# Kernel tuning notes

Hardware: AMD Instinct MI355X
Metric: run time of the kernel (lower is better)

The kernel has to match this reference:

```python
import jax, jax.numpy as jnp
import numpy as np

B, S, D, H = 2, 2048, 1024, 16
DK = D // H  # 64


def setup_inputs() -> dict:
    key = jax.random.key(0)
    ks = jax.random.split(key, 4)
    scale = 1.0 / np.sqrt(D)
    return {
        "q_input": jax.random.normal(ks[0], (B, S, D), dtype=jnp.float32),
        "W_q": jax.random.normal(ks[1], (D, D), dtype=jnp.float32) * scale,
        "b_q": jnp.zeros((D,), dtype=jnp.float32),
        "W_k": jax.random.normal(ks[2], (D, D), dtype=jnp.float32) * scale,
        "b_k": jnp.zeros((D,), dtype=jnp.float32),
        "W_v": jax.random.normal(ks[3], (D, D), dtype=jnp.float32) * scale,
        "b_v": jnp.zeros((D,), dtype=jnp.float32),
    }


def reference(q_input, W_q, b_q, W_k, b_k, W_v, b_v):
    # Self-attention: k_input and v_input default to q_input in the torch module.
    # nn.Linear computes x @ W.T + b
    q = q_input @ W_q.T + b_q
    k = q_input @ W_k.T + b_k
    v = q_input @ W_v.T + b_v

    # [B,S,D] -> [B,H,S,DK]
    def split_heads(x):
        return x.reshape(B, S, H, DK).transpose(0, 2, 1, 3)

    qh, kh, vh = split_heads(q), split_heads(k), split_heads(v)

    # scores [B,H,S,S]; causal mask added BEFORE scaling (as in source; -inf invariant)
    scores = jnp.einsum("bhqd,bhkd->bhqk", qh, kh)
    causal = jnp.tril(jnp.ones((S, S), dtype=bool))
    scores = jnp.where(causal[None, None], scores, -jnp.inf)
    scores = scores / jnp.sqrt(jnp.float32(DK))
    probs = jax.nn.softmax(scores, axis=-1)
    z = jnp.einsum("bhqk,bhkd->bhqd", probs, vh)  # [B,H,S,DK]
    # [B,H,S,DK] -> [B,S,H,DK] -> [B,S,D]
    return z.transpose(0, 2, 1, 3).reshape(B, S, D)
```

## Files before the change

kernel.cpp:

```cpp
#include <hip/hip_runtime.h>
#include <hip/hip_bf16.h>
#include <stdint.h>

typedef __attribute__((ext_vector_type(8))) short short8;
typedef __attribute__((ext_vector_type(4))) short short4v;
typedef __attribute__((ext_vector_type(4))) float f32x4;

#define B_ 2
#define S_ 2048
#define D_ 1024
#define H_ 16
#define DK_ 64
#define M_ (B_*S_)

#define WS_QKV   0
#define WS_XB    12582912
#define WS_WB    16777216

#define QSCALE (0.125f * 1.44269504088896f)

#define GLL16(g, l) __builtin_amdgcn_global_load_lds( \
    (const __attribute__((address_space(1))) void*)(g), \
    (__attribute__((address_space(3))) void*)(l), 16, 0, 0)

#define WAIT_VM0 asm volatile("s_waitcnt vmcnt(0)" ::: "memory")
#define WAIT_VM4 asm volatile("s_waitcnt vmcnt(4)" ::: "memory")
#define BARRIER_RAW asm volatile("s_barrier" ::: "memory")

static __device__ __forceinline__ short f2bf(float f){
  union { float f; unsigned u; } x; x.f = f;
  unsigned r = x.u + 0x7fff + ((x.u >> 16) & 1);
  return (short)(r >> 16);
}

__global__ __launch_bounds__(256) void cvt_bf16(
    const float* __restrict__ X,  const float* __restrict__ Wq,
    const float* __restrict__ Wk, const float* __restrict__ Wv,
    short* __restrict__ ws)
{
  const int z = blockIdx.z;
  const float* src; short* dst; int n;
  if (z == 0)      { src = X;  dst = ws + WS_XB;               n = M_*D_; }
  else if (z == 1) { src = Wq; dst = ws + WS_WB;               n = D_*D_; }
  else if (z == 2) { src = Wk; dst = ws + WS_WB + D_*D_;       n = D_*D_; }
  else             { src = Wv; dst = ws + WS_WB + 2*(D_*D_);   n = D_*D_; }
  const int stride = gridDim.x * blockDim.x * 4;
  for (int i = (blockIdx.x * blockDim.x + threadIdx.x) * 4; i < n; i += stride) {
    float4 v = *(const float4*)(src + i);
    short4v o;
    o.x = f2bf(v.x); o.y = f2bf(v.y); o.z = f2bf(v.z); o.w = f2bf(v.w);
    *(short4v*)(dst + i) = o;
  }
}

__global__ __launch_bounds__(256, 3) void qkv_gemm(
    const short* __restrict__ ws_in,
    const float* __restrict__ bq, const float* __restrict__ bk,
    const float* __restrict__ bv, short* __restrict__ qkv)
{
  const int z = blockIdx.z;
  const short* X  = ws_in + WS_XB;
  const short* Wm = ws_in + WS_WB + (size_t)z * (D_*D_);
  const float* bias = (z==0) ? bq : (z==1) ? bk : bv;
  short* out = qkv + (size_t)z * (M_*D_);

  __shared__ short lds[24576];

  const int t = threadIdx.x;
  const int w = t >> 6, lane = t & 63;
  const int quad = lane >> 4, l16 = lane & 15;
  const int wm = w & 1, wn = w >> 1;
  const int m0 = blockIdx.y * 128, n0 = blockIdx.x * 128;

  const int lr = lane >> 2, lc = lane & 3;
  const int csrc = lc ^ (lr & 3);
  const size_t arow0 = (size_t)(m0 + w*16     + lr) * D_ + csrc*8;
  const size_t arow1 = (size_t)(m0 + (w+4)*16 + lr) * D_ + csrc*8;
  const size_t brow0 = (size_t)(n0 + w*16     + lr) * D_ + csrc*8;
  const size_t brow1 = (size_t)(n0 + (w+4)*16 + lr) * D_ + csrc*8;

  f32x4 acc[4][4];
  #pragma unroll
  for (int i=0;i<4;i++)
    #pragma unroll
    for (int j=0;j<4;j++) acc[i][j] = (f32x4){0.f,0.f,0.f,0.f};

  #pragma unroll
  for (int p=0;p<2;p++){
    GLL16(X  + arow0 + p*32, lds + p*4096 + (w*16)*32);
    GLL16(X  + arow1 + p*32, lds + p*4096 + ((w+4)*16)*32);
    GLL16(Wm + brow0 + p*32, lds + 12288 + p*4096 + (w*16)*32);
    GLL16(Wm + brow1 + p*32, lds + 12288 + p*4096 + ((w+4)*16)*32);
  }

  const int ca = quad ^ (l16 & 3);
  int cur = 0;
  for (int kk = 0; kk < 32; kk++) {
    if (kk < 31) { WAIT_VM4; }
    else         { WAIT_VM0; }
    BARRIER_RAW;
    if (kk < 30) {
      int slot = cur + 2; if (slot >= 3) slot -= 3;
      const int ko = (kk+2)*32;
      short* An = lds + slot*4096;
      short* Bn = lds + 12288 + slot*4096;
      GLL16(X  + arow0 + ko, An + (w*16)*32);
      GLL16(X  + arow1 + ko, An + ((w+4)*16)*32);
      GLL16(Wm + brow0 + ko, Bn + (w*16)*32);
      GLL16(Wm + brow1 + ko, Bn + ((w+4)*16)*32);
    }
    const short* Ac = lds + cur*4096;
    const short* Bc = lds + 12288 + cur*4096;
    short8 af[4], bfr[4];
    #pragma unroll
    for (int mt=0;mt<4;mt++)
      af[mt] = *(const short8*)(Ac + (wm*64 + mt*16 + l16)*32 + ca*8);
    #pragma unroll
    for (int nt=0;nt<4;nt++)
      bfr[nt] = *(const short8*)(Bc + (wn*64 + nt*16 + l16)*32 + ca*8);
    if (z != 2) {
      #pragma unroll
      for (int mt=0;mt<4;mt++)
        #pragma unroll
        for (int nt=0;nt<4;nt++)
          acc[mt][nt] = __builtin_amdgcn_mfma_f32_16x16x32_bf16(af[mt], bfr[nt], acc[mt][nt], 0,0,0);
    } else {
      #pragma unroll
      for (int nt=0;nt<4;nt++)
        #pragma unroll
        for (int mt=0;mt<4;mt++)
          acc[nt][mt] = __builtin_amdgcn_mfma_f32_16x16x32_bf16(bfr[nt], af[mt], acc[nt][mt], 0,0,0);
    }
    cur = (cur==2) ? 0 : cur+1;
  }

  __syncthreads();

  if (z != 2) {
    const float scale = (z==0) ? QSCALE : 1.0f;
    #pragma unroll
    for (int nt=0;nt<4;nt++){
      const int col_l = wn*64 + nt*16 + l16;
      const float bvv = bias[n0 + col_l];
      #pragma unroll
      for (int mt=0;mt<4;mt++)
        #pragma unroll
        for (int i=0;i<4;i++){
          const int row_l = wm*64 + mt*16 + quad*4 + i;
          lds[row_l*136 + col_l] = f2bf((acc[mt][nt][i] + bvv) * scale);
        }
    }
    __syncthreads();
    #pragma unroll
    for (int k=0;k<8;k++){
      const int cid = k*256 + t;
      const int row = cid >> 4, cc = cid & 15;
      short8 vv = *(const short8*)(lds + row*136 + cc*8);
      const int m = m0 + row, bidx = m >> 11, s = m & 2047;
      const int n = n0 + cc*8, h = n >> 6, dd = n & 63;
      *(short8*)(out + (((size_t)(bidx*H_ + h))*S_ + s)*DK_ + dd) = vv;
    }
  } else {
    #pragma unroll
    for (int nt=0;nt<4;nt++)
      #pragma unroll
      for (int i=0;i<4;i++){
        const int n_l = wn*64 + nt*16 + quad*4 + i;
        const float bvv = bias[n0 + n_l];
        #pragma unroll
        for (int mt=0;mt<4;mt++){
          const int m_l = wm*64 + mt*16 + l16;
          lds[n_l*136 + m_l] = f2bf(acc[nt][mt][i] + bvv);
        }
      }
    __syncthreads();
    #pragma unroll
    for (int k=0;k<8;k++){
      const int cid = k*256 + t;
      const int rowN = cid >> 4, cc = cid & 15;
      short8 vv = *(const short8*)(lds + rowN*136 + cc*8);
      const int n = n0 + rowN, h = n >> 6, dd = n & 63;
      const int m = m0 + cc*8, bidx = m >> 11, s0 = m & 2047;
      *(short8*)(out + (((size_t)(bidx*H_ + h))*DK_ + dd)*S_ + s0) = vv;
    }
  }
}

__global__ __launch_bounds__(256, 2) void attn(
    const short* __restrict__ qkv, float* __restrict__ out)
{
  const int bh = blockIdx.y;
  const int qt = (gridDim.x - 1) - blockIdx.x;
  const short* Q  = qkv + (size_t)bh * (S_*DK_);
  const short* K  = Q + (size_t)(M_*D_);
  const short* VT = qkv + (size_t)(2*M_*D_) + (size_t)bh * (DK_*S_);

  __shared__ short Qs[8192];
  __shared__ short Kbuf[2][4096];
  __shared__ short Vbuf[2][4096];
  __shared__ short Ps[8192];

  const int t = threadIdx.x;
  const int w = t >> 6, lane = t & 63;
  const int quad = lane >> 4, l16 = lane & 15;
  const int sw = l16 & 7;
  const int lr = lane >> 3, lc = lane & 7;
  const int csrc = lc ^ lr;

  #pragma unroll
  for (int p=0;p<4;p++){
    const int rb = (p*4 + w)*8;
    GLL16(Q + (size_t)(qt*128 + rb + lr)*DK_ + csrc*8, Qs + rb*64);
  }
  #pragma unroll
  for (int j=0;j<2;j++){
    const int rb = (j*4 + w)*8;
    GLL16(K  + (size_t)(rb + lr)*DK_ + csrc*8, &Kbuf[0][0] + rb*64);
    GLL16(VT + (size_t)(rb + lr)*S_  + csrc*8, &Vbuf[0][0] + rb*64);
  }

  f32x4 o[2][4];
  float lsum[2];
  #pragma unroll
  for (int mt=0;mt<2;mt++){
    #pragma unroll
    for (int nd=0;nd<4;nd++) o[mt][nd] = (f32x4){0.f,0.f,0.f,0.f};
    lsum[mt] = 0.f;
  }

  short8 bq[2][2];
  const int nkt = 2*qt + 2;
  int cur = 0;
  const int pw_half = (quad & 1) * 4;
  const int pw_ckb  = quad >> 1;

  for (int kt = 0; kt < nkt; kt++){
    WAIT_VM0;
    BARRIER_RAW;
    const int nxt = cur ^ 1;
    if (kt + 1 < nkt) {
      const int kb2 = (kt+1)*64;
      short* Kn = &Kbuf[nxt][0];
      short* Vn = &Vbuf[nxt][0];
      #pragma unroll
      for (int j=0;j<2;j++){
        const int rb = (j*4 + w)*8;
        GLL16(K  + (size_t)(kb2 + rb + lr)*DK_ + csrc*8, Kn + rb*64);
        GLL16(VT + (size_t)(rb + lr)*S_ + kb2 + csrc*8,  Vn + rb*64);
      }
    }
    if (kt == 0) {
      #pragma unroll
      for (int kc=0;kc<2;kc++){
        const int xch = (kc*4 + quad) ^ sw;
        #pragma unroll
        for (int mt=0;mt<2;mt++)
          bq[kc][mt] = *(const short8*)(Qs + (w*32 + mt*16 + l16)*64 + xch*8);
      }
    }
    const short* Kc = &Kbuf[cur][0];
    const short* Vc = &Vbuf[cur][0];
    const int kb = kt*64;

    f32x4 sc[4][2];
    #pragma unroll
    for (int ntk=0;ntk<4;ntk++)
      #pragma unroll
      for (int mt=0;mt<2;mt++) sc[ntk][mt] = (f32x4){0.f,0.f,0.f,0.f};
    #pragma unroll
    for (int kc=0;kc<2;kc++){
      const int xch = (kc*4 + quad) ^ sw;
      short8 ak[4];
      #pragma unroll
      for (int ntk=0;ntk<4;ntk++)
        ak[ntk] = *(const short8*)(Kc + (ntk*16 + l16)*64 + xch*8);
      #pragma unroll
      for (int ntk=0;ntk<4;ntk++)
        #pragma unroll
        for (int mt=0;mt<2;mt++)
          sc[ntk][mt] = __builtin_amdgcn_mfma_f32_16x16x32_bf16(ak[ntk], bq[kc][mt], sc[ntk][mt], 0,0,0);
    }

    const int q0w = qt*128 + w*32;
    if (kb + 63 > q0w) {
      #pragma unroll
      for (int ntk=0;ntk<4;ntk++)
        #pragma unroll
        for (int mt=0;mt<2;mt++){
          const int qg = q0w + mt*16 + l16;
          #pragma unroll
          for (int i=0;i<4;i++){
            const int kg = kb + ntk*16 + quad*4 + i;
            if (kg > qg) sc[ntk][mt][i] = -3.0e38f;
          }
        }
    }

    #pragma unroll
    for (int mt=0;mt<2;mt++){
      const int r = w*32 + mt*16 + l16;
      #pragma unroll
      for (int ntk=0;ntk<4;ntk++){
        float p0 = __builtin_amdgcn_exp2f(sc[ntk][mt][0]);
        float p1 = __builtin_amdgcn_exp2f(sc[ntk][mt][1]);
        float p2 = __builtin_amdgcn_exp2f(sc[ntk][mt][2]);
        float p3 = __builtin_amdgcn_exp2f(sc[ntk][mt][3]);
        lsum[mt] += (p0+p1) + (p2+p3);
        short4v pk;
        pk.x = f2bf(p0); pk.y = f2bf(p1); pk.z = f2bf(p2); pk.w = f2bf(p3);
        const int slot = (ntk*2 + pw_ckb) ^ sw;
        *(short4v*)(Ps + r*64 + slot*8 + pw_half) = pk;
      }
    }
    asm volatile("" ::: "memory");

    #pragma unroll
    for (int kc=0;kc<2;kc++){
      const int xch = (kc*4 + quad) ^ sw;
      short8 pa[2], vb[4];
      #pragma unroll
      for (int mt=0;mt<2;mt++)
        pa[mt] = *(const short8*)(Ps + (w*32 + mt*16 + l16)*64 + xch*8);
      #pragma unroll
      for (int nd=0;nd<4;nd++)
        vb[nd] = *(const short8*)(Vc + (nd*16 + l16)*64 + xch*8);
      #pragma unroll
      for (int mt=0;mt<2;mt++)
        #pragma unroll
        for (int nd=0;nd<4;nd++)
          o[mt][nd] = __builtin_amdgcn_mfma_f32_16x16x32_bf16(pa[mt], vb[nd], o[mt][nd], 0,0,0);
    }
    cur = nxt;
  }

  const int bb = bh >> 4, h = bh & 15;
  float linv[2];
  #pragma unroll
  for (int mt=0;mt<2;mt++){
    float rs = lsum[mt];
    rs += __shfl_xor(rs, 16, 64);
    rs += __shfl_xor(rs, 32, 64);
    linv[mt] = 1.0f / rs;
  }
  #pragma unroll
  for (int mt=0;mt<2;mt++){
    #pragma unroll
    for (int i=0;i<4;i++){
      const float lw = __shfl(linv[mt], (quad<<4) + (quad<<2) + i, 64);
      const int q = qt*128 + w*32 + mt*16 + quad*4 + i;
      #pragma unroll
      for (int nd=0;nd<4;nd++){
        const int d = nd*16 + l16;
        out[ ((size_t)bb*S_ + q)*D_ + h*DK_ + d ] = o[mt][nd][i] * lw;
      }
    }
  }
}

extern "C" void kernel_launch(void* const* d_in, const int* in_sizes, int n_in,
                              void* d_out, int out_size, void* d_ws, size_t ws_size,
                              hipStream_t stream)
{
  (void)in_sizes; (void)n_in; (void)out_size; (void)ws_size;
  const float* X  = (const float*)d_in[0];
  const float* Wq = (const float*)d_in[1];
  const float* bq = (const float*)d_in[2];
  const float* Wk = (const float*)d_in[3];
  const float* bk = (const float*)d_in[4];
  const float* Wv = (const float*)d_in[5];
  const float* bv = (const float*)d_in[6];
  short* ws  = (short*)d_ws;
  float* out = (float*)d_out;

  dim3 g0(1024, 1, 4);
  cvt_bf16<<<g0, dim3(256,1,1), 0, stream>>>(X, Wq, Wk, Wv, ws);
  dim3 g1(D_/128, M_/128, 3);
  qkv_gemm<<<g1, dim3(256,1,1), 0, stream>>>(ws, bq, bk, bv, ws + WS_QKV);
  dim3 g2(S_/128, B_*H_);
  attn<<<g2, dim3(256,1,1), 0, stream>>>(ws + WS_QKV, out);
}
```

Measured before the change: 187.0 us.

## Split long causal attention rows across two blocks with atomic merge

The attention kernel now launches 24 work items per head instead of 16. For query tiles 8-15 the key range is split into two chunks of at most 16 key tiles, and the ranks are ordered so the longest work runs first. Split blocks atomically add unnormalized outputs and row sums into zeroed fp32 accumulators, and the last block to arrive normalizes and writes the result. The K/V staging also moves from double to triple buffering with a deeper prefetch. This adds a zeroing kernel, atomic traffic and reuse of workspace, in exchange for better load balance across the causal triangle.

```diff
diff --git a/kernel.cpp b/kernel.cpp
--- a/kernel.cpp
+++ b/kernel.cpp
@@ -32,6 +32,9 @@
   unsigned r = x.u + 0x7fff + ((x.u >> 16) & 1);
   return (short)(r >> 16);
 }
+
+__constant__ signed char QT_TAB[24] = {15,15,14,13,12,11,10,9,8,7,14,6,13,5,12,4,11,3,10,2,9,1,8,0};
+__constant__ signed char C_TAB[24]  = { 0, 1, 0, 0, 0, 0, 0,0,0,0, 1,0, 1,0, 1,0, 1,0, 1,0,1,0,1,0};
 
 __global__ __launch_bounds__(256) void cvt_bf16(
     const float* __restrict__ X,  const float* __restrict__ Wq,
@@ -186,19 +189,41 @@
   }
 }
 
+__global__ __launch_bounds__(256) void zero_acc(float* __restrict__ Oacc,
+                                                float* __restrict__ LT)
+{
+  const int i = blockIdx.x * 256 + threadIdx.x;
+  if (i < 524288) {
+    ((float4*)Oacc)[i] = make_float4(0.f,0.f,0.f,0.f);
+  } else {
+    const int j = i - 524288;
+    if (j < 8256) ((float4*)LT)[j] = make_float4(0.f,0.f,0.f,0.f);
+  }
+}
+
 __global__ __launch_bounds__(256, 2) void attn(
-    const short* __restrict__ qkv, float* __restrict__ out)
+    const short* __restrict__ qkv, float* __restrict__ Oacc,
+    float* __restrict__ Lacc, int* __restrict__ tick,
+    float* __restrict__ out)
 {
-  const int bh = blockIdx.y;
-  const int qt = (gridDim.x - 1) - blockIdx.x;
+  const int bh = blockIdx.x;
+  const int rank = blockIdx.y;
+  const int qt = QT_TAB[rank];
+  const int c  = C_TAB[rank];
+  const int nkt = 2*qt + 2;
+  const int kt0 = c*16;
+  const int kt1 = (kt0 + 16 < nkt) ? kt0 + 16 : nkt;
+  const bool split = (qt >= 8);
+
   const short* Q  = qkv + (size_t)bh * (S_*DK_);
   const short* K  = Q + (size_t)(M_*D_);
   const short* VT = qkv + (size_t)(2*M_*D_) + (size_t)bh * (DK_*S_);
 
   __shared__ short Qs[8192];
-  __shared__ short Kbuf[2][4096];
-  __shared__ short Vbuf[2][4096];
+  __shared__ short Kbuf[3][4096];
+  __shared__ short Vbuf[3][4096];
   __shared__ short Ps[8192];
+  __shared__ int sflag;
 
   const int t = threadIdx.x;
   const int w = t >> 6, lane = t & 63;
@@ -213,10 +238,14 @@
     GLL16(Q + (size_t)(qt*128 + rb + lr)*DK_ + csrc*8, Qs + rb*64);
   }
   #pragma unroll
-  for (int j=0;j<2;j++){
-    const int rb = (j*4 + w)*8;
-    GLL16(K  + (size_t)(rb + lr)*DK_ + csrc*8, &Kbuf[0][0] + rb*64);
-    GLL16(VT + (size_t)(rb + lr)*S_  + csrc*8, &Vbuf[0][0] + rb*64);
+  for (int p=0;p<2;p++){
+    const int kb = (kt0 + p)*64;
+    #pragma unroll
+    for (int j=0;j<2;j++){
+      const int rb = (j*4 + w)*8;
+      GLL16(K  + (size_t)(kb + rb + lr)*DK_ + csrc*8, &Kbuf[p][0] + rb*64);
+      GLL16(VT + (size_t)(rb + lr)*S_ + kb  + csrc*8, &Vbuf[p][0] + rb*64);
+    }
   }
 
   f32x4 o[2][4];
@@ -229,19 +258,18 @@
   }
 
   short8 bq[2][2];
-  const int nkt = 2*qt + 2;
-  int cur = 0;
   const int pw_half = (quad & 1) * 4;
   const int pw_ckb  = quad >> 1;
 
-  for (int kt = 0; kt < nkt; kt++){
-    WAIT_VM0;
+  for (int kt = kt0; kt < kt1; kt++){
+    if (kt == kt1-1) { WAIT_VM0; } else { WAIT_VM4; }
     BARRIER_RAW;
-    const int nxt = cur ^ 1;
-    if (kt + 1 < nkt) {
-      const int kb2 = (kt+1)*64;
-      short* Kn = &Kbuf[nxt][0];
-      short* Vn = &Vbuf[nxt][0];
+    const int bi = (kt - kt0) % 3;
+    if (kt + 2 < kt1) {
+      int slot = bi + 2; if (slot >= 3) slot -= 3;
+      const int kb2 = (kt+2)*64;
+      short* Kn = &Kbuf[slot][0];
+      short* Vn = &Vbuf[slot][0];
       #pragma unroll
       for (int j=0;j<2;j++){
         const int rb = (j*4 + w)*8;
@@ -249,7 +277,7 @@
         GLL16(VT + (size_t)(rb + lr)*S_ + kb2 + csrc*8,  Vn + rb*64);
       }
     }
-    if (kt == 0) {
+    if (kt == kt0) {
       #pragma unroll
       for (int kc=0;kc<2;kc++){
         const int xch = (kc*4 + quad) ^ sw;
@@ -258,8 +286,8 @@
           bq[kc][mt] = *(const short8*)(Qs + (w*32 + mt*16 + l16)*64 + xch*8);
       }
     }
-    const short* Kc = &Kbuf[cur][0];
-    const short* Vc = &Vbuf[cur][0];
+    const short* Kc = &Kbuf[bi][0];
+    const short* Vc = &Vbuf[bi][0];
     const int kb = kt*64;
 
     f32x4 sc[4][2];
@@ -330,29 +358,66 @@
         for (int nd=0;nd<4;nd++)
           o[mt][nd] = __builtin_amdgcn_mfma_f32_16x16x32_bf16(pa[mt], vb[nd], o[mt][nd], 0,0,0);
     }
-    cur = nxt;
   }
 
   const int bb = bh >> 4, h = bh & 15;
-  float linv[2];
+
+  if (!split) {
+    float linv[2];
+    #pragma unroll
+    for (int mt=0;mt<2;mt++){
+      float rs = lsum[mt];
+      rs += __shfl_xor(rs, 16, 64);
+      rs += __shfl_xor(rs, 32, 64);
+      linv[mt] = 1.0f / rs;
+    }
+    #pragma unroll
+    for (int mt=0;mt<2;mt++){
+      #pragma unroll
+      for (int i=0;i<4;i++){
+        const float lw = __shfl(linv[mt], (quad<<4) + (quad<<2) + i, 64);
+        const int q = qt*128 + w*32 + mt*16 + quad*4 + i;
+        #pragma unroll
+        for (int nd=0;nd<4;nd++){
+          const int d = nd*16 + l16;
+          out[ ((size_t)bb*S_ + q)*D_ + h*DK_ + d ] = o[mt][nd][i] * lw;
+        }
+      }
+    }
+    return;
+  }
+
+  const int qb = qt*128 - 1024;
   #pragma unroll
   for (int mt=0;mt<2;mt++){
     float rs = lsum[mt];
     rs += __shfl_xor(rs, 16, 64);
     rs += __shfl_xor(rs, 32, 64);
-    linv[mt] = 1.0f / rs;
-  }
-  #pragma unroll
-  for (int mt=0;mt<2;mt++){
-    #pragma unroll
-    for (int i=0;i<4;i++){
-      const float lw = __shfl(linv[mt], (quad<<4) + (quad<<2) + i, 64);
-      const int q = qt*128 + w*32 + mt*16 + quad*4 + i;
-      #pragma unroll
-      for (int nd=0;nd<4;nd++){
+    if (quad == 0)
+      atomicAdd(&Lacc[bh*1024 + qb + w*32 + mt*16 + l16], rs);
+  }
+  #pragma unroll
+  for (int mt=0;mt<2;mt++)
+    #pragma unroll
+    for (int nd=0;nd<4;nd++)
+      #pragma unroll
+      for (int i=0;i<4;i++){
+        const int q_l = w*32 + mt*16 + quad*4 + i;
         const int d = nd*16 + l16;
-        out[ ((size_t)bb*S_ + q)*D_ + h*DK_ + d ] = o[mt][nd][i] * lw;
-      }
+        atomicAdd(&Oacc[(size_t)(bh*1024 + qb + q_l)*64 + d], o[mt][nd][i]);
+      }
+
+  __threadfence();
+  __syncthreads();
+  if (t == 0) sflag = atomicAdd(&tick[bh*8 + (qt-8)], 1);
+  __syncthreads();
+  if (sflag == 1) {
+    __threadfence();
+    for (int idx = t; idx < 8192; idx += 256) {
+      const int q_l = idx >> 6, d = idx & 63;
+      const float l = Lacc[bh*1024 + qb + q_l];
+      const float v = Oacc[(size_t)(bh*1024 + qb + q_l)*64 + d];
+      out[ ((size_t)bb*S_ + qt*128 + q_l)*D_ + h*DK_ + d ] = v / l;
     }
   }
 }
@@ -372,10 +437,15 @@
   short* ws  = (short*)d_ws;
   float* out = (float*)d_out;
 
+  float* Oacc = (float*)(ws + WS_XB);
+  float* Lacc = (float*)(ws + WS_WB);
+  int*   tick = (int*)(Lacc + 32*1024);
+
   dim3 g0(1024, 1, 4);
   cvt_bf16<<<g0, dim3(256,1,1), 0, stream>>>(X, Wq, Wk, Wv, ws);
   dim3 g1(D_/128, M_/128, 3);
   qkv_gemm<<<g1, dim3(256,1,1), 0, stream>>>(ws, bq, bk, bv, ws + WS_QKV);
-  dim3 g2(S_/128, B_*H_);
-  attn<<<g2, dim3(256,1,1), 0, stream>>>(ws + WS_QKV, out);
-}
+  zero_acc<<<dim3(2081,1,1), dim3(256,1,1), 0, stream>>>(Oacc, Lacc);
+  dim3 g2(B_*H_, 24);
+  attn<<<g2, dim3(256,1,1), 0, stream>>>(ws + WS_QKV, Oacc, Lacc, tick, out);
+}
```

After: 263.1 us. +40.7%, slower.
